# Kernel optimization log

Hardware: AMD Instinct MI355X
Metric: run time of the kernel (lower is better)

The kernel has to match this reference:

```python
import jax, jax.numpy as jnp
import numpy as np


def _fft_feats(x):
    # x: [B, 3, H, W] float32
    B, C, H, W = x.shape
    gray = 0.299 * x[:, 0] + 0.587 * x[:, 1] + 0.114 * x[:, 2]  # [B,H,W]
    mag = jnp.abs(jnp.fft.fftshift(jnp.fft.fft2(gray), axes=(-2, -1))) + 1e-8
    mag = mag / (mag.max(axis=(-2, -1), keepdims=True) + 1e-8)
    m = mag.reshape(B, -1)
    n = m.shape[1]
    mean = m.mean(axis=1)
    std = jnp.clip(jnp.std(m, axis=1, ddof=1), 1e-8, None)  # torch unbiased std
    mx = m.max(axis=1)
    mn = m.min(axis=1)
    gt_mean = (m > mean[:, None]).astype(jnp.float32).mean(axis=1)
    # torch.median returns the lower of the two middle values for even n
    med = jnp.sort(m, axis=1)[:, (n - 1) // 2]
    q1 = mag[:, : H // 4].mean(axis=(1, 2))
    q2 = mag[:, H // 4 : H // 2].mean(axis=(1, 2))
    q3 = mag[:, H // 2 : 3 * H // 4].mean(axis=(1, 2))
    q4 = mag[:, 3 * H // 4 :].mean(axis=(1, 2))
    gt_half = (m > 0.5).astype(jnp.float32).mean(axis=1)
    gt_tenth = (m > 0.1).astype(jnp.float32).mean(axis=1)
    feats = jnp.stack([mean, std, mx, mn, gt_mean, med, q1, q2, q3, q4, gt_half, gt_tenth], axis=1)
    return jnp.clip(feats, -10.0, 10.0)  # [B,12]


def _bn(h, gamma, beta):
    # BatchNorm1d, training-mode forward (batch statistics, biased var), eps=1e-5
    mu = h.mean(axis=0)
    var = h.var(axis=0)
    return gamma * (h - mu) / jnp.sqrt(var + 1e-5) + beta


def _mlp(f, W1, b1, g1, be1, W2, b2, g2, be2, W3, b3):
    h = jax.nn.relu(_bn(f @ W1 + b1, g1, be1))  # Dropout(0.1) treated as identity (eval)
    h = jax.nn.relu(_bn(h @ W2 + b2, g2, be2))
    return h @ W3 + b3


def setup_inputs() -> dict:
    key = jax.random.key(0)
    ks = jax.random.split(key, 8)
    B, H, W = 64, 512, 512
    D = 512  # output_dim
    x = jax.random.normal(ks[0], (B, 3, H, W), dtype=jnp.float32)
    W1 = jax.random.normal(ks[1], (12, 64), dtype=jnp.float32) * 0.2
    b1 = jnp.zeros((64,), jnp.float32)
    g1 = jnp.ones((64,), jnp.float32)
    be1 = jnp.zeros((64,), jnp.float32)
    W2 = jax.random.normal(ks[2], (64, 128), dtype=jnp.float32) * 0.1
    b2 = jnp.zeros((128,), jnp.float32)
    g2 = jnp.ones((128,), jnp.float32)
    be2 = jnp.zeros((128,), jnp.float32)
    W3 = jax.random.normal(ks[3], (128, D), dtype=jnp.float32) * 0.08
    b3 = jnp.zeros((D,), jnp.float32)
    return {"x": x, "W1": W1, "b1": b1, "g1": g1, "be1": be1,
            "W2": W2, "b2": b2, "g2": g2, "be2": be2, "W3": W3, "b3": b3}


def reference(x, W1, b1, g1, be1, W2, b2, g2, be2, W3, b3):
    feats = _fft_feats(x)
    return _mlp(feats, W1, b1, g1, be1, W2, b2, g2, be2, W3, b3)
```

## Files before the change

### kernel.cpp

```cpp
#include <hip/hip_runtime.h>
#include <math.h>

#ifndef M_PI
#define M_PI 3.14159265358979323846
#endif

#define BB 64
#define HH 512
#define WW 512
#define NPIX (HH*WW)
#define MED_K 131072u
#define WS 260
#define PADI(i) ((i) + ((i) >> 5))

__device__ __forceinline__ float2 cmulf(float2 a, float2 b){
  return make_float2(a.x*b.x - a.y*b.y, a.x*b.y + a.y*b.x);
}
__device__ __forceinline__ unsigned rev9(unsigned v){ return __brev(v) >> 23; }

__device__ __forceinline__ double wred_add(double v){
  #pragma unroll
  for (int o = 32; o > 0; o >>= 1) v += __shfl_down(v, o, 64);
  return v;
}
__device__ __forceinline__ float wred_min(float v){
  #pragma unroll
  for (int o = 32; o > 0; o >>= 1) v = fminf(v, __shfl_down(v, o, 64));
  return v;
}
__device__ __forceinline__ float wred_max(float v){
  #pragma unroll
  for (int o = 32; o > 0; o >>= 1) v = fmaxf(v, __shfl_down(v, o, 64));
  return v;
}
__device__ __forceinline__ unsigned wred_addu(unsigned v){
  #pragma unroll
  for (int o = 32; o > 0; o >>= 1) v += __shfl_down(v, o, 64);
  return v;
}
__device__ __forceinline__ float wred_add_all(float v){
  #pragma unroll
  for (int o = 32; o > 0; o >>= 1) v += __shfl_xor(v, o, 64);
  return v;
}

__global__ void twiddle_init_kernel(float2* __restrict__ twg){
  int t = threadIdx.x;
  double a = -2.0 * M_PI * (double)t / 512.0;
  twg[t] = make_float2((float)cos(a), (float)sin(a));
}

__global__ __launch_bounds__(256) void row_fft_kernel(const float* __restrict__ x,
                                                      const float2* __restrict__ twg,
                                                      float2* __restrict__ out){
  __shared__ float sre[528], sim[528];
  __shared__ float2 tw[256];
  int t = threadIdx.x;
  tw[t] = twg[t];
  int pair = blockIdx.x;
  int b = pair >> 8, hp = pair & 255;
  const float* base = x + (size_t)b*3*NPIX + (size_t)(2*hp)*WW;
  int rsel = t >> 7;
  int f4i = t & 127;
  const float* rowbase = base + rsel*WW;
  float4 rv = ((const float4*)rowbase)[f4i];
  float4 gv = ((const float4*)(rowbase + NPIX))[f4i];
  float4 bv = ((const float4*)(rowbase + 2*NPIX))[f4i];
  float g[4] = {0.299f*rv.x + 0.587f*gv.x + 0.114f*bv.x,
                0.299f*rv.y + 0.587f*gv.y + 0.114f*bv.y,
                0.299f*rv.z + 0.587f*gv.z + 0.114f*bv.z,
                0.299f*rv.w + 0.587f*gv.w + 0.114f*bv.w};
  int col0 = f4i << 2;
  #pragma unroll
  for (int q = 0; q < 4; ++q){
    int p = PADI((int)rev9((unsigned)(col0 + q)));
    if (rsel == 0) sre[p] = g[q]; else sim[p] = g[q];
  }
  __syncthreads();
  #pragma unroll
  for (int st = 1; st <= 9; ++st){
    int half = 1 << (st-1);
    int k = t & (half - 1);
    int i1 = ((t >> (st-1)) << st) + k;
    int i2 = i1 + half;
    int p1 = PADI(i1), p2 = PADI(i2);
    float2 w = tw[k << (9 - st)];
    float2 u = make_float2(sre[p1], sim[p1]);
    float2 raw = make_float2(sre[p2], sim[p2]);
    float2 v = cmulf(w, raw);
    sre[p1] = u.x + v.x; sim[p1] = u.y + v.y;
    sre[p2] = u.x - v.x; sim[p2] = u.y - v.y;
    __syncthreads();
  }
  int row0 = (b << 9) + 2*hp;
  float2* o0 = out + (size_t)row0*WW;
  float2* o1 = o0 + WW;
  #pragma unroll
  for (int kk = 0; kk < 2; ++kk){
    int k = t + (kk << 8);
    if (k > 256) continue;
    int mk = (512 - k) & 511;
    int pk = PADI(k), pmk = PADI(mk);
    float zr = sre[pk], zi = sim[pk];
    float wr = sre[pmk], wi = sim[pmk];
    o0[k] = make_float2(0.5f*(zr + wr), 0.5f*(zi - wi));
    o1[k] = make_float2(0.5f*(zi + wi), 0.5f*(wr - zr));
  }
}

__global__ __launch_bounds__(512) void col_fft_kernel(const float2* __restrict__ in,
    const float2* __restrict__ twg,
    float* __restrict__ magc,
    unsigned* __restrict__ dmax, unsigned* __restrict__ dmin,
    double* __restrict__ sum, double* __restrict__ sumsq, double* __restrict__ qsum,
    unsigned* __restrict__ hist1)
{
  __shared__ float2 s[512*16];
  __shared__ float2 tw[256];
  __shared__ unsigned h[2048];
  __shared__ double bufd[6][8];
  __shared__ float buff[2][8];
  int t = threadIdx.x;
  if (t < 256) tw[t] = twg[t];
  for (int i = t; i < 2048; i += 512) h[i] = 0;
  int b = blockIdx.x / 17;
  int j0 = (blockIdx.x % 17) << 4;
  const float2* base = in + (size_t)b*NPIX;
  for (int idx = t; idx < 512*16; idx += 512){
    int e = idx >> 4, c = idx & 15;
    int j = j0 + c;
    float2 v = (j <= 256) ? base[(size_t)e*WW + j] : make_float2(0.f, 0.f);
    s[(int)rev9((unsigned)e)*16 + c] = v;
  }
  __syncthreads();
  #pragma unroll
  for (int st = 1; st <= 9; ++st){
    int half = 1 << (st-1);
    #pragma unroll
    for (int qq = 0; qq < 8; ++qq){
      int tt = t + (qq << 9);
      int c = tt & 15;
      int kk = tt >> 4;
      int k = kk & (half - 1);
      int i1 = ((kk >> (st-1)) << st) + k;
      int i2 = i1 + half;
      float2 w = tw[k << (9 - st)];
      float2 u = s[i1*16 + c];
      float2 v = cmulf(w, s[i2*16 + c]);
      s[i1*16 + c] = make_float2(u.x + v.x, u.y + v.y);
      s[i2*16 + c] = make_float2(u.x - v.x, u.y - v.y);
    }
    __syncthreads();
  }
  double lsum=0.0, lsq=0.0, lq0=0.0, lq1=0.0, lq2=0.0, lq3=0.0;
  float lmn = 3.4e38f, lmx = 0.f;
  float* mo = magc + (size_t)b*(512*WS);
  for (int idx = t; idx < 512*16; idx += 512){
    int e = idx >> 4, c = idx & 15;
    int j = j0 + c;
    if (j > 256) continue;
    float2 v = s[e*16 + c];
    float m = sqrtf(v.x*v.x + v.y*v.y) + 1e-8f;
    int si = (e + 256) & 511;
    mo[(size_t)si*WS + j] = m;
    unsigned w = (j == 0 || j == 256) ? 1u : 2u;
    double md = (double)m;
    double wm = (w == 2u) ? md + md : md;
    lsum += wm;
    lsq  += wm * md;
    lmn = fminf(lmn, m); lmx = fmaxf(lmx, m);
    atomicAdd(&h[__float_as_uint(m) >> 20], w);
    int qa = si >> 7;
    lq0 += (qa==0)?md:0.0; lq1 += (qa==1)?md:0.0; lq2 += (qa==2)?md:0.0; lq3 += (qa==3)?md:0.0;
    if (w == 2u){
      int qb = ((512 - si) & 511) >> 7;
      lq0 += (qb==0)?md:0.0; lq1 += (qb==1)?md:0.0; lq2 += (qb==2)?md:0.0; lq3 += (qb==3)?md:0.0;
    }
  }
  int lane = t & 63, wv = t >> 6;
  double r0 = wred_add(lsum), r1 = wred_add(lsq);
  double r2 = wred_add(lq0), r3 = wred_add(lq1), r4 = wred_add(lq2), r5 = wred_add(lq3);
  float fmn = wred_min(lmn), fmx = wred_max(lmx);
  if (lane == 0){
    bufd[0][wv]=r0; bufd[1][wv]=r1; bufd[2][wv]=r2;
    bufd[3][wv]=r3; bufd[4][wv]=r4; bufd[5][wv]=r5;
    buff[0][wv]=fmn; buff[1][wv]=fmx;
  }
  __syncthreads();
  if (t == 0){
    double s0=0,s1=0,s2=0,s3=0,s4=0,s5=0; float mn=3.4e38f, mx=0.f;
    for (int i = 0; i < 8; ++i){
      s0+=bufd[0][i]; s1+=bufd[1][i]; s2+=bufd[2][i];
      s3+=bufd[3][i]; s4+=bufd[4][i]; s5+=bufd[5][i];
      mn=fminf(mn,buff[0][i]); mx=fmaxf(mx,buff[1][i]);
    }
    atomicAdd(sum + b, s0);
    atomicAdd(sumsq + b, s1);
    atomicAdd(qsum + b*4 + 0, s2);
    atomicAdd(qsum + b*4 + 1, s3);
    atomicAdd(qsum + b*4 + 2, s4);
    atomicAdd(qsum + b*4 + 3, s5);
    atomicMin(dmin + b, __float_as_uint(mn));
    atomicMax(dmax + b, __float_as_uint(mx));
  }
  unsigned* hb = hist1 + (size_t)b*2048;
  for (int i = t; i < 2048; i += 512){
    unsigned c = h[i];
    if (c) atomicAdd(&hb[i], c);
  }
}

__global__ void scan1_kernel(const unsigned* __restrict__ hist,
                             unsigned* __restrict__ sel, unsigned* __restrict__ rem){
  int b = blockIdx.x;
  const unsigned* hb = hist + (size_t)b*2048;
  __shared__ unsigned part[256];
  int t = threadIdx.x;
  unsigned s = 0;
  for (int i = 0; i < 8; ++i) s += hb[t*8 + i];
  part[t] = s; __syncthreads();
  if (t == 0){
    unsigned target = MED_K, cum = 0; int seg = 0;
    for (; seg < 256; ++seg){ if (cum + part[seg] >= target) break; cum += part[seg]; }
    unsigned r = target - cum;
    int bin = seg*8;
    for (;; ++bin){ unsigned c = hb[bin]; if (c >= r) break; r -= c; }
    sel[b] = (unsigned)bin;
    rem[b] = r;
  }
}

__global__ __launch_bounds__(256) void pass2_kernel(const float4* __restrict__ magc4,
    const unsigned* __restrict__ sel1, const double* __restrict__ sum,
    const unsigned* __restrict__ dmax,
    unsigned* __restrict__ hist2, unsigned* __restrict__ cnt_gtm,
    unsigned* __restrict__ cnt_half, unsigned* __restrict__ cnt_tenth)
{
  __shared__ unsigned h[16384];
  __shared__ unsigned rb[3][8];
  int t = threadIdx.x, b = blockIdx.x;
  for (int i = t; i < 16384; i += 256) h[i] = 0;
  __syncthreads();
  unsigned s1 = sel1[b];
  float meanf = (float)(sum[b] / (double)NPIX);
  float d = __uint_as_float(dmax[b]) + 1e-8f;
  float th = 0.5f*d, tl = 0.1f*d;
  const float4* p = magc4 + (size_t)b*(512*(WS/4)) + (size_t)blockIdx.y*128*(WS/4);
  unsigned lgm = 0, lh = 0, lt = 0;
  for (int idx = t; idx < 128*(WS/4); idx += 256){
    float4 v = p[idx];
    int k = idx % (WS/4);
    int jc0 = k*4;
    float a[4] = {v.x, v.y, v.z, v.w};
    #pragma unroll
    for (int q = 0; q < 4; ++q){
      int jc = jc0 + q;
      if (jc > 256) continue;
      unsigned w = (jc == 0 || jc == 256) ? 1u : 2u;
      float m = a[q];
      unsigned bits = __float_as_uint(m);
      if ((bits >> 20) == s1) atomicAdd(&h[(bits >> 6) & 0x3fffu], w);
      lgm += (m > meanf) ? w : 0u;
      lh  += (m > th) ? w : 0u;
      lt  += (m > tl) ? w : 0u;
    }
  }
  int lane = t & 63, wv = t >> 6;
  unsigned g0 = wred_addu(lgm), g1 = wred_addu(lh), g2 = wred_addu(lt);
  if (lane == 0){ rb[0][wv]=g0; rb[1][wv]=g1; rb[2][wv]=g2; }
  __syncthreads();
  if (t == 0){
    unsigned a0=0,a1=0,a2=0;
    for (int i = 0; i < 4; ++i){ a0+=rb[0][i]; a1+=rb[1][i]; a2+=rb[2][i]; }
    atomicAdd(cnt_gtm + b, a0);
    atomicAdd(cnt_half + b, a1);
    atomicAdd(cnt_tenth + b, a2);
  }
  unsigned* hb = hist2 + (size_t)b*16384;
  for (int i = t; i < 16384; i += 256){
    unsigned c = h[i];
    if (c) atomicAdd(&hb[i], c);
  }
}

__global__ void scan2_kernel(const unsigned* __restrict__ hist,
    const unsigned* __restrict__ sel1, const unsigned* __restrict__ rem1,
    unsigned* __restrict__ medbits){
  int b = blockIdx.x;
  const unsigned* hb = hist + (size_t)b*16384;
  __shared__ unsigned part[256];
  int t = threadIdx.x;
  unsigned s = 0;
  for (int i = 0; i < 64; ++i) s += hb[t*64 + i];
  part[t] = s; __syncthreads();
  if (t == 0){
    unsigned target = rem1[b], cum = 0; int seg = 0;
    for (; seg < 256; ++seg){ if (cum + part[seg] >= target) break; cum += part[seg]; }
    unsigned r = target - cum;
    int bin = seg*64;
    for (;; ++bin){ unsigned c = hb[bin]; if (c >= r) break; r -= c; }
    medbits[b] = (sel1[b] << 20) | ((unsigned)bin << 6) | 32u;
  }
}

__global__ void feats_kernel(const unsigned* __restrict__ dmax, const unsigned* __restrict__ dmin,
    const double* __restrict__ sum, const double* __restrict__ sumsq, const double* __restrict__ qsum,
    const unsigned* __restrict__ cnt_half, const unsigned* __restrict__ cnt_tenth,
    const unsigned* __restrict__ cnt_gtmean, const unsigned* __restrict__ medbits,
    float* __restrict__ feats)
{
  int b = threadIdx.x;
  if (b >= BB) return;
  float maxv = __uint_as_float(dmax[b]);
  float d = maxv + 1e-8f;
  double dd = (double)d;
  double n = (double)NPIX;
  double sm = sum[b] / dd;
  double sq = sumsq[b] / (dd*dd);
  double mean = sm / n;
  double var = (sq - sm*sm/n) / (n - 1.0);
  if (var < 0.0) var = 0.0;
  float stdv = (float)sqrt(var);
  if (stdv < 1e-8f) stdv = 1e-8f;
  float mx = maxv / d;
  float mn = __uint_as_float(dmin[b]) / d;
  float gtm = (float)((double)cnt_gtmean[b] / n);
  float med = __uint_as_float(medbits[b]) / d;
  float q0 = (float)(qsum[b*4+0] / dd * (1.0/65536.0));
  float q1 = (float)(qsum[b*4+1] / dd * (1.0/65536.0));
  float q2 = (float)(qsum[b*4+2] / dd * (1.0/65536.0));
  float q3 = (float)(qsum[b*4+3] / dd * (1.0/65536.0));
  float gh = (float)((double)cnt_half[b] / n);
  float gt = (float)((double)cnt_tenth[b] / n);
  float f[12] = {(float)mean, stdv, mx, mn, gtm, med, q0, q1, q2, q3, gh, gt};
  #pragma unroll
  for (int i = 0; i < 12; ++i){
    float v = f[i];
    v = fminf(fmaxf(v, -10.f), 10.f);
    feats[b*12 + i] = v;
  }
}

__global__ __launch_bounds__(64) void mlp1_kernel(const float* __restrict__ feats,
    const float* __restrict__ W1, const float* __restrict__ b1,
    const float* __restrict__ g1, const float* __restrict__ be1,
    float* __restrict__ h1t)
{
  int c = blockIdx.x, r = threadIdx.x;
  float acc = b1[c];
  #pragma unroll
  for (int k = 0; k < 12; ++k) acc += feats[r*12 + k] * W1[k*64 + c];
  float mu = wred_add_all(acc) * (1.f/BB);
  float dv = acc - mu;
  float var = wred_add_all(dv*dv) * (1.f/BB);
  float scv = g1[c] / sqrtf(var + 1e-5f);
  float v = dv*scv + be1[c];
  h1t[c*BB + r] = v > 0.f ? v : 0.f;
}

__global__ __launch_bounds__(64) void mlp2_kernel(const float* __restrict__ h1t,
    const float* __restrict__ W2, const float* __restrict__ b2,
    const float* __restrict__ g2, const float* __restrict__ be2,
    float* __restrict__ h2t)
{
  int c = blockIdx.x, r = threadIdx.x;
  float acc = b2[c];
  #pragma unroll 4
  for (int k = 0; k < 64; ++k) acc += h1t[k*BB + r] * W2[k*128 + c];
  float mu = wred_add_all(acc) * (1.f/BB);
  float dv = acc - mu;
  float var = wred_add_all(dv*dv) * (1.f/BB);
  float scv = g2[c] / sqrtf(var + 1e-5f);
  float v = dv*scv + be2[c];
  h2t[c*BB + r] = v > 0.f ? v : 0.f;
}

__global__ __launch_bounds__(256) void mlp3_kernel(const float* __restrict__ h2t,
    const float* __restrict__ W3, const float* __restrict__ b3,
    float* __restrict__ out)
{
  int r = threadIdx.x & 63;
  int w = threadIdx.x >> 6;
  int c = blockIdx.x*4 + w;
  float acc = b3[c];
  #pragma unroll 4
  for (int k = 0; k < 128; ++k) acc += h2t[k*BB + r] * W3[k*512 + c];
  out[r*512 + c] = acc;
}

extern "C" void kernel_launch(void* const* d_in, const int* in_sizes, int n_in,
                              void* d_out, int out_size, void* d_ws, size_t ws_size,
                              hipStream_t stream) {
  (void)in_sizes; (void)n_in; (void)out_size; (void)ws_size;
  const float* x   = (const float*)d_in[0];
  const float* W1  = (const float*)d_in[1];
  const float* b1  = (const float*)d_in[2];
  const float* g1  = (const float*)d_in[3];
  const float* be1 = (const float*)d_in[4];
  const float* W2  = (const float*)d_in[5];
  const float* b2  = (const float*)d_in[6];
  const float* g2  = (const float*)d_in[7];
  const float* be2 = (const float*)d_in[8];
  const float* W3  = (const float*)d_in[9];
  const float* b3  = (const float*)d_in[10];
  float* out = (float*)d_out;

  char* ws = (char*)d_ws;
  float2* bufc = (float2*)ws;
  float*  magc = (float*)(ws + 134217728);
  unsigned* hist1 = (unsigned*)(ws + 134217728 + 34078720);
  unsigned* hist2 = (unsigned*)(ws + 168296448 + 524288);
  char* sc = ws + 168820736 + 4194304;
  unsigned* dmax      = (unsigned*)(sc + 0);
  unsigned* dmin      = (unsigned*)(sc + 256);
  double*   sum       = (double*)(sc + 512);
  double*   sumsq     = (double*)(sc + 1024);
  double*   qsum      = (double*)(sc + 1536);
  unsigned* cnt_half  = (unsigned*)(sc + 3584);
  unsigned* cnt_tenth = (unsigned*)(sc + 3840);
  unsigned* cnt_gtm   = (unsigned*)(sc + 4096);
  unsigned* sel1      = (unsigned*)(sc + 4352);
  unsigned* rem1      = (unsigned*)(sc + 4608);
  unsigned* medbits   = (unsigned*)(sc + 4864);
  float*    feats     = (float*)(sc + 5120);
  float*    h1t       = (float*)(sc + 8192);
  float*    h2t       = (float*)(sc + 8192 + 16384);
  float2*   twg       = (float2*)(sc + 8192 + 16384 + 32768);

  hipMemsetAsync(hist1, 0, 524288 + 4194304, stream);
  hipMemsetAsync(sc, 0, 8192, stream);
  hipMemsetAsync(dmin, 0xFF, 256, stream);

  twiddle_init_kernel<<<1, 256, 0, stream>>>(twg);
  row_fft_kernel<<<BB*256, 256, 0, stream>>>(x, twg, bufc);
  col_fft_kernel<<<BB*17, 512, 0, stream>>>(bufc, twg, magc, dmax, dmin, sum, sumsq, qsum, hist1);
  scan1_kernel<<<BB, 256, 0, stream>>>(hist1, sel1, rem1);
  pass2_kernel<<<dim3(BB, 4), 256, 0, stream>>>((const float4*)magc, sel1, sum, dmax,
      hist2, cnt_gtm, cnt_half, cnt_tenth);
  scan2_kernel<<<BB, 256, 0, stream>>>(hist2, sel1, rem1, medbits);
  feats_kernel<<<1, 64, 0, stream>>>(dmax, dmin, sum, sumsq, qsum, cnt_half, cnt_tenth, cnt_gtm, medbits, feats);
  mlp1_kernel<<<64, 64, 0, stream>>>(feats, W1, b1, g1, be1, h1t);
  mlp2_kernel<<<128, 64, 0, stream>>>(h1t, W2, b2, g2, be2, h2t);
  mlp3_kernel<<<128, 256, 0, stream>>>(h2t, W3, b3, out);
}
```

Baseline: 469.3 us.

## Fuse scan kernels into consumers, fold memsets into init, use float partial sums

Removes the scan1 and feats kernels by recomputing the coarse-histogram median selection inside pass2 and inside a merged scan2+features kernel. The two scalar memsets are replaced by writes in the twiddle init kernel. The column FFT kernel's per-thread accumulators and wave reductions move from double to float, keeping double only for the final per-block combine, which cuts FP64 work at some cost in accuracy. Each pass2 block now redoes the histogram scan, adding a little redundant work per block.

```diff
diff --git a/kernel.cpp b/kernel.cpp
--- a/kernel.cpp
+++ b/kernel.cpp
@@ -18,7 +18,7 @@
 }
 __device__ __forceinline__ unsigned rev9(unsigned v){ return __brev(v) >> 23; }
 
-__device__ __forceinline__ double wred_add(double v){
+__device__ __forceinline__ float wredf(float v){
   #pragma unroll
   for (int o = 32; o > 0; o >>= 1) v += __shfl_down(v, o, 64);
   return v;
@@ -44,10 +44,15 @@
   return v;
 }
 
-__global__ void twiddle_init_kernel(float2* __restrict__ twg){
+__global__ void init_kernel(float2* __restrict__ twg, unsigned* __restrict__ scal){
   int t = threadIdx.x;
   double a = -2.0 * M_PI * (double)t / 512.0;
   twg[t] = make_float2((float)cos(a), (float)sin(a));
+  #pragma unroll
+  for (int q = 0; q < 8; ++q){
+    int w = t*8 + q;
+    scal[w] = (w >= 64 && w < 128) ? 0xFFFFFFFFu : 0u;
+  }
 }
 
 __global__ __launch_bounds__(256) void row_fft_kernel(const float* __restrict__ x,
@@ -118,8 +123,7 @@
   __shared__ float2 s[512*16];
   __shared__ float2 tw[256];
   __shared__ unsigned h[2048];
-  __shared__ double bufd[6][8];
-  __shared__ float buff[2][8];
+  __shared__ float buff[8][8];
   int t = threadIdx.x;
   if (t < 256) tw[t] = twg[t];
   for (int i = t; i < 2048; i += 512) h[i] = 0;
@@ -152,7 +156,7 @@
     }
     __syncthreads();
   }
-  double lsum=0.0, lsq=0.0, lq0=0.0, lq1=0.0, lq2=0.0, lq3=0.0;
+  float lsum=0.f, lsq=0.f, lq0=0.f, lq1=0.f, lq2=0.f, lq3=0.f;
   float lmn = 3.4e38f, lmx = 0.f;
   float* mo = magc + (size_t)b*(512*WS);
   for (int idx = t; idx < 512*16; idx += 512){
@@ -164,35 +168,34 @@
     int si = (e + 256) & 511;
     mo[(size_t)si*WS + j] = m;
     unsigned w = (j == 0 || j == 256) ? 1u : 2u;
-    double md = (double)m;
-    double wm = (w == 2u) ? md + md : md;
+    float wm = (w == 2u) ? m + m : m;
     lsum += wm;
-    lsq  += wm * md;
+    lsq = fmaf(wm, m, lsq);
     lmn = fminf(lmn, m); lmx = fmaxf(lmx, m);
     atomicAdd(&h[__float_as_uint(m) >> 20], w);
     int qa = si >> 7;
-    lq0 += (qa==0)?md:0.0; lq1 += (qa==1)?md:0.0; lq2 += (qa==2)?md:0.0; lq3 += (qa==3)?md:0.0;
+    lq0 += (qa==0)?m:0.f; lq1 += (qa==1)?m:0.f; lq2 += (qa==2)?m:0.f; lq3 += (qa==3)?m:0.f;
     if (w == 2u){
-      int qb = ((512 - si) & 511) >> 7;
-      lq0 += (qb==0)?md:0.0; lq1 += (qb==1)?md:0.0; lq2 += (qb==2)?md:0.0; lq3 += (qb==3)?md:0.0;
+      int qb = si ? 3 - ((si-1) >> 7) : 0;
+      lq0 += (qb==0)?m:0.f; lq1 += (qb==1)?m:0.f; lq2 += (qb==2)?m:0.f; lq3 += (qb==3)?m:0.f;
     }
   }
   int lane = t & 63, wv = t >> 6;
-  double r0 = wred_add(lsum), r1 = wred_add(lsq);
-  double r2 = wred_add(lq0), r3 = wred_add(lq1), r4 = wred_add(lq2), r5 = wred_add(lq3);
+  float r0 = wredf(lsum), r1 = wredf(lsq);
+  float r2 = wredf(lq0), r3 = wredf(lq1), r4 = wredf(lq2), r5 = wredf(lq3);
   float fmn = wred_min(lmn), fmx = wred_max(lmx);
   if (lane == 0){
-    bufd[0][wv]=r0; bufd[1][wv]=r1; bufd[2][wv]=r2;
-    bufd[3][wv]=r3; bufd[4][wv]=r4; bufd[5][wv]=r5;
-    buff[0][wv]=fmn; buff[1][wv]=fmx;
+    buff[0][wv]=r0; buff[1][wv]=r1; buff[2][wv]=r2;
+    buff[3][wv]=r3; buff[4][wv]=r4; buff[5][wv]=r5;
+    buff[6][wv]=fmn; buff[7][wv]=fmx;
   }
   __syncthreads();
   if (t == 0){
     double s0=0,s1=0,s2=0,s3=0,s4=0,s5=0; float mn=3.4e38f, mx=0.f;
     for (int i = 0; i < 8; ++i){
-      s0+=bufd[0][i]; s1+=bufd[1][i]; s2+=bufd[2][i];
-      s3+=bufd[3][i]; s4+=bufd[4][i]; s5+=bufd[5][i];
-      mn=fminf(mn,buff[0][i]); mx=fmaxf(mx,buff[1][i]);
+      s0+=(double)buff[0][i]; s1+=(double)buff[1][i]; s2+=(double)buff[2][i];
+      s3+=(double)buff[3][i]; s4+=(double)buff[4][i]; s5+=(double)buff[5][i];
+      mn=fminf(mn,buff[6][i]); mx=fmaxf(mx,buff[7][i]);
     }
     atomicAdd(sum + b, s0);
     atomicAdd(sumsq + b, s1);
@@ -210,38 +213,36 @@
   }
 }
 
-__global__ void scan1_kernel(const unsigned* __restrict__ hist,
-                             unsigned* __restrict__ sel, unsigned* __restrict__ rem){
-  int b = blockIdx.x;
-  const unsigned* hb = hist + (size_t)b*2048;
+__global__ __launch_bounds__(256) void pass2_kernel(const float4* __restrict__ magc4,
+    const unsigned* __restrict__ hist1, const double* __restrict__ sum,
+    const unsigned* __restrict__ dmax,
+    unsigned* __restrict__ hist2, unsigned* __restrict__ cnt_gtm,
+    unsigned* __restrict__ cnt_half, unsigned* __restrict__ cnt_tenth)
+{
+  __shared__ unsigned h[16384];
   __shared__ unsigned part[256];
-  int t = threadIdx.x;
-  unsigned s = 0;
-  for (int i = 0; i < 8; ++i) s += hb[t*8 + i];
-  part[t] = s; __syncthreads();
+  __shared__ unsigned rb[3][8];
+  __shared__ unsigned s_sel;
+  int t = threadIdx.x, b = blockIdx.x;
+  for (int i = t; i < 16384; i += 256) h[i] = 0;
+  const unsigned* hb1 = hist1 + (size_t)b*2048;
+  {
+    unsigned sp = 0;
+    #pragma unroll
+    for (int i = 0; i < 8; ++i) sp += hb1[t*8 + i];
+    part[t] = sp;
+  }
+  __syncthreads();
   if (t == 0){
     unsigned target = MED_K, cum = 0; int seg = 0;
     for (; seg < 256; ++seg){ if (cum + part[seg] >= target) break; cum += part[seg]; }
     unsigned r = target - cum;
     int bin = seg*8;
-    for (;; ++bin){ unsigned c = hb[bin]; if (c >= r) break; r -= c; }
-    sel[b] = (unsigned)bin;
-    rem[b] = r;
-  }
-}
-
-__global__ __launch_bounds__(256) void pass2_kernel(const float4* __restrict__ magc4,
-    const unsigned* __restrict__ sel1, const double* __restrict__ sum,
-    const unsigned* __restrict__ dmax,
-    unsigned* __restrict__ hist2, unsigned* __restrict__ cnt_gtm,
-    unsigned* __restrict__ cnt_half, unsigned* __restrict__ cnt_tenth)
-{
-  __shared__ unsigned h[16384];
-  __shared__ unsigned rb[3][8];
-  int t = threadIdx.x, b = blockIdx.x;
-  for (int i = t; i < 16384; i += 256) h[i] = 0;
-  __syncthreads();
-  unsigned s1 = sel1[b];
+    for (;; ++bin){ unsigned c = hb1[bin]; if (c >= r) break; r -= c; }
+    s_sel = (unsigned)bin;
+  }
+  __syncthreads();
+  unsigned s1 = s_sel;
   float meanf = (float)(sum[b] / (double)NPIX);
   float d = __uint_as_float(dmax[b]) + 1e-8f;
   float th = 0.5f*d, tl = 0.1f*d;
@@ -283,61 +284,76 @@
   }
 }
 
-__global__ void scan2_kernel(const unsigned* __restrict__ hist,
-    const unsigned* __restrict__ sel1, const unsigned* __restrict__ rem1,
-    unsigned* __restrict__ medbits){
-  int b = blockIdx.x;
-  const unsigned* hb = hist + (size_t)b*16384;
+__global__ __launch_bounds__(256) void scan2_feats_kernel(
+    const unsigned* __restrict__ hist1, const unsigned* __restrict__ hist2,
+    const unsigned* __restrict__ dmax, const unsigned* __restrict__ dmin,
+    const double* __restrict__ sum, const double* __restrict__ sumsq,
+    const double* __restrict__ qsum,
+    const unsigned* __restrict__ cnt_half, const unsigned* __restrict__ cnt_tenth,
+    const unsigned* __restrict__ cnt_gtmean,
+    float* __restrict__ feats)
+{
+  int b = blockIdx.x, t = threadIdx.x;
   __shared__ unsigned part[256];
-  int t = threadIdx.x;
-  unsigned s = 0;
-  for (int i = 0; i < 64; ++i) s += hb[t*64 + i];
-  part[t] = s; __syncthreads();
+  __shared__ unsigned s_sel, s_rem;
+  const unsigned* hb1 = hist1 + (size_t)b*2048;
+  {
+    unsigned sp = 0;
+    #pragma unroll
+    for (int i = 0; i < 8; ++i) sp += hb1[t*8 + i];
+    part[t] = sp;
+  }
+  __syncthreads();
   if (t == 0){
-    unsigned target = rem1[b], cum = 0; int seg = 0;
+    unsigned target = MED_K, cum = 0; int seg = 0;
+    for (; seg < 256; ++seg){ if (cum + part[seg] >= target) break; cum += part[seg]; }
+    unsigned r = target - cum;
+    int bin = seg*8;
+    for (;; ++bin){ unsigned c = hb1[bin]; if (c >= r) break; r -= c; }
+    s_sel = (unsigned)bin; s_rem = r;
+  }
+  __syncthreads();
+  const unsigned* hb2 = hist2 + (size_t)b*16384;
+  {
+    unsigned sp = 0;
+    for (int i = 0; i < 64; ++i) sp += hb2[t*64 + i];
+    part[t] = sp;
+  }
+  __syncthreads();
+  if (t == 0){
+    unsigned target = s_rem, cum = 0; int seg = 0;
     for (; seg < 256; ++seg){ if (cum + part[seg] >= target) break; cum += part[seg]; }
     unsigned r = target - cum;
     int bin = seg*64;
-    for (;; ++bin){ unsigned c = hb[bin]; if (c >= r) break; r -= c; }
-    medbits[b] = (sel1[b] << 20) | ((unsigned)bin << 6) | 32u;
-  }
-}
-
-__global__ void feats_kernel(const unsigned* __restrict__ dmax, const unsigned* __restrict__ dmin,
-    const double* __restrict__ sum, const double* __restrict__ sumsq, const double* __restrict__ qsum,
-    const unsigned* __restrict__ cnt_half, const unsigned* __restrict__ cnt_tenth,
-    const unsigned* __restrict__ cnt_gtmean, const unsigned* __restrict__ medbits,
-    float* __restrict__ feats)
-{
-  int b = threadIdx.x;
-  if (b >= BB) return;
-  float maxv = __uint_as_float(dmax[b]);
-  float d = maxv + 1e-8f;
-  double dd = (double)d;
-  double n = (double)NPIX;
-  double sm = sum[b] / dd;
-  double sq = sumsq[b] / (dd*dd);
-  double mean = sm / n;
-  double var = (sq - sm*sm/n) / (n - 1.0);
-  if (var < 0.0) var = 0.0;
-  float stdv = (float)sqrt(var);
-  if (stdv < 1e-8f) stdv = 1e-8f;
-  float mx = maxv / d;
-  float mn = __uint_as_float(dmin[b]) / d;
-  float gtm = (float)((double)cnt_gtmean[b] / n);
-  float med = __uint_as_float(medbits[b]) / d;
-  float q0 = (float)(qsum[b*4+0] / dd * (1.0/65536.0));
-  float q1 = (float)(qsum[b*4+1] / dd * (1.0/65536.0));
-  float q2 = (float)(qsum[b*4+2] / dd * (1.0/65536.0));
-  float q3 = (float)(qsum[b*4+3] / dd * (1.0/65536.0));
-  float gh = (float)((double)cnt_half[b] / n);
-  float gt = (float)((double)cnt_tenth[b] / n);
-  float f[12] = {(float)mean, stdv, mx, mn, gtm, med, q0, q1, q2, q3, gh, gt};
-  #pragma unroll
-  for (int i = 0; i < 12; ++i){
-    float v = f[i];
-    v = fminf(fmaxf(v, -10.f), 10.f);
-    feats[b*12 + i] = v;
+    for (;; ++bin){ unsigned c = hb2[bin]; if (c >= r) break; r -= c; }
+    unsigned medbits = (s_sel << 20) | ((unsigned)bin << 6) | 32u;
+    float maxv = __uint_as_float(dmax[b]);
+    float dd_f = maxv + 1e-8f;
+    double dd = (double)dd_f;
+    double n = (double)NPIX;
+    double sm = sum[b] / dd;
+    double sq = sumsq[b] / (dd*dd);
+    double mean = sm / n;
+    double var = (sq - sm*sm/n) / (n - 1.0);
+    if (var < 0.0) var = 0.0;
+    float stdv = (float)sqrt(var);
+    if (stdv < 1e-8f) stdv = 1e-8f;
+    float f[12];
+    f[0] = (float)mean;
+    f[1] = stdv;
+    f[2] = maxv / dd_f;
+    f[3] = __uint_as_float(dmin[b]) / dd_f;
+    f[4] = (float)((double)cnt_gtmean[b] / n);
+    f[5] = __uint_as_float(medbits) / dd_f;
+    f[6] = (float)(qsum[b*4+0] / dd * (1.0/65536.0));
+    f[7] = (float)(qsum[b*4+1] / dd * (1.0/65536.0));
+    f[8] = (float)(qsum[b*4+2] / dd * (1.0/65536.0));
+    f[9] = (float)(qsum[b*4+3] / dd * (1.0/65536.0));
+    f[10] = (float)((double)cnt_half[b] / n);
+    f[11] = (float)((double)cnt_tenth[b] / n);
+    #pragma unroll
+    for (int i = 0; i < 12; ++i)
+      feats[b*12 + i] = fminf(fmaxf(f[i], -10.f), 10.f);
   }
 }
 
@@ -419,26 +435,20 @@
   unsigned* cnt_half  = (unsigned*)(sc + 3584);
   unsigned* cnt_tenth = (unsigned*)(sc + 3840);
   unsigned* cnt_gtm   = (unsigned*)(sc + 4096);
-  unsigned* sel1      = (unsigned*)(sc + 4352);
-  unsigned* rem1      = (unsigned*)(sc + 4608);
-  unsigned* medbits   = (unsigned*)(sc + 4864);
   float*    feats     = (float*)(sc + 5120);
   float*    h1t       = (float*)(sc + 8192);
   float*    h2t       = (float*)(sc + 8192 + 16384);
   float2*   twg       = (float2*)(sc + 8192 + 16384 + 32768);
 
   hipMemsetAsync(hist1, 0, 524288 + 4194304, stream);
-  hipMemsetAsync(sc, 0, 8192, stream);
-  hipMemsetAsync(dmin, 0xFF, 256, stream);
-
-  twiddle_init_kernel<<<1, 256, 0, stream>>>(twg);
+
+  init_kernel<<<1, 256, 0, stream>>>(twg, (unsigned*)sc);
   row_fft_kernel<<<BB*256, 256, 0, stream>>>(x, twg, bufc);
   col_fft_kernel<<<BB*17, 512, 0, stream>>>(bufc, twg, magc, dmax, dmin, sum, sumsq, qsum, hist1);
-  scan1_kernel<<<BB, 256, 0, stream>>>(hist1, sel1, rem1);
-  pass2_kernel<<<dim3(BB, 4), 256, 0, stream>>>((const float4*)magc, sel1, sum, dmax,
+  pass2_kernel<<<dim3(BB, 4), 256, 0, stream>>>((const float4*)magc, hist1, sum, dmax,
       hist2, cnt_gtm, cnt_half, cnt_tenth);
-  scan2_kernel<<<BB, 256, 0, stream>>>(hist2, sel1, rem1, medbits);
-  feats_kernel<<<1, 64, 0, stream>>>(dmax, dmin, sum, sumsq, qsum, cnt_half, cnt_tenth, cnt_gtm, medbits, feats);
+  scan2_feats_kernel<<<BB, 256, 0, stream>>>(hist1, hist2, dmax, dmin, sum, sumsq, qsum,
+      cnt_half, cnt_tenth, cnt_gtm, feats);
   mlp1_kernel<<<64, 64, 0, stream>>>(feats, W1, b1, g1, be1, h1t);
   mlp2_kernel<<<128, 64, 0, stream>>>(h1t, W2, b2, g2, be2, h2t);
   mlp3_kernel<<<128, 256, 0, stream>>>(h2t, W3, b3, out);
```

After: 469.0 us. Within noise of the previous version (-0.1%).
